# Optimization experiments

Hardware: AMD Instinct MI355X
Metric: run time of the kernel (lower is better)

Reference implementation:

```python
import jax, jax.numpy as jnp
import numpy as np

HID = 512
VOCAB = 2048
K_CB = 4


def conv1d(x, w, b, stride):
    # x: [B, C_in, L], w: [C_out, C_in, 7], torch Conv1d(k=7, stride, pad=3)
    y = jax.lax.conv_general_dilated(
        x, w, window_strides=(stride,), padding=[(3, 3)],
        dimension_numbers=("NCH", "OIH", "NCH"))
    return y + b[None, :, None]


def setup_inputs() -> dict:
    key = jax.random.key(0)
    ks = jax.random.split(key, 9)
    B, S = 4, 32768
    audio = jax.random.normal(ks[0], (B, 1, S), dtype=jnp.float32)
    # encoder params (fan-in scaled init, like torch default scale-wise)
    w1 = jax.random.normal(ks[1], (HID // 4, 1, 7), dtype=jnp.float32) * (1.0 / np.sqrt(1 * 7))
    b1 = jnp.zeros((HID // 4,), dtype=jnp.float32)
    w2 = jax.random.normal(ks[2], (HID // 2, HID // 4, 7), dtype=jnp.float32) * (1.0 / np.sqrt(HID // 4 * 7))
    b2 = jnp.zeros((HID // 2,), dtype=jnp.float32)
    w3 = jax.random.normal(ks[3], (HID, HID // 2, 7), dtype=jnp.float32) * (1.0 / np.sqrt(HID // 2 * 7))
    b3 = jnp.zeros((HID,), dtype=jnp.float32)
    codebook = jax.random.normal(ks[4], (K_CB, VOCAB, HID), dtype=jnp.float32)
    embedding = jax.random.normal(ks[5], (VOCAB, HID), dtype=jnp.float32)
    return {"audio": audio, "w1": w1, "b1": b1, "w2": w2, "b2": b2,
            "w3": w3, "b3": b3, "codebook": codebook, "embedding": embedding}


def reference(audio, w1, b1, w2, b2, w3, b3, codebook, embedding):
    # conv encoder: [B,1,S] -> [B,H,L], L = S/8
    f = jax.nn.relu(conv1d(audio, w1, b1, 2))
    f = jax.nn.relu(conv1d(f, w2, b2, 2))
    f = conv1d(f, w3, b3, 2)
    feats = jnp.transpose(f, (0, 2, 1))  # [B, L, H]

    # multi-codebook nearest neighbor: argmin of squared L2 == argmin of cdist
    f2 = jnp.sum(feats * feats, axis=-1)          # [B, L]
    c2 = jnp.sum(codebook * codebook, axis=-1)    # [K, V]
    cross = jnp.einsum("blh,kvh->bklv", feats, codebook)  # [B, K, L, V]
    d2 = f2[:, None, :, None] + c2[None, :, None, :] - 2.0 * cross
    tokens = jnp.argmin(d2, axis=-1)              # [B, K, L] (stack over codebooks at dim=1)
    emb = embedding[tokens].mean(axis=1)          # [B, L, H]
    return tokens, emb
```

## Files before the change

### kernel.cpp

```cpp
#include <hip/hip_runtime.h>
#include <hip/hip_bf16.h>
#include <stdint.h>

#define B_ 4
#define S_IN 32768
#define C1V 128
#define L1V 16384
#define C2V 256
#define L2V 8192
#define C3V 512
#define L3V 4096
#define VOCABV 2048
#define KCB 4

#define R1P (2 * (L1V + 16))
#define P1P (L1V + 16)
#define R2P (2 * (L2V + 16))
#define P2P (L2V + 16)

typedef _Float16 half8 __attribute__((ext_vector_type(8)));
typedef float floatx4 __attribute__((ext_vector_type(4)));

#define AS1 __attribute__((address_space(1)))
#define AS3 __attribute__((address_space(3)))

__device__ __forceinline__ void gload_lds16(const void* g, void* l) {
    __builtin_amdgcn_global_load_lds((const AS1 void*)g, (AS3 void*)l, 16, 0, 0);
}

__device__ __forceinline__ half8 lds_read_half8_a4(const _Float16* p) {
    union { uint32_t u[4]; half8 h; } t;
    const uint32_t* w = (const uint32_t*)p;
    t.u[0] = w[0]; t.u[1] = w[1]; t.u[2] = w[2]; t.u[3] = w[3];
    return t.h;
}

__global__ void padzero_kernel(_Float16* __restrict__ x1h, _Float16* __restrict__ x2h) {
    int j = blockIdx.x * 256 + threadIdx.x;
    half8 z;
#pragma unroll
    for (int i = 0; i < 8; ++i) z[i] = (_Float16)0.f;
    if (j < 2048) {
        int row = j >> 2, p = j & 3;
        size_t base = (size_t)row * R1P + (size_t)(p >> 1) * P1P + ((p & 1) ? (L1V + 8) : 0);
        *(half8*)(x1h + base) = z;
    } else if (j < 6144) {
        int j2 = j - 2048;
        int row = j2 >> 2, p = j2 & 3;
        size_t base = (size_t)row * R2P + (size_t)(p >> 1) * P2P + ((p & 1) ? (L2V + 8) : 0);
        *(half8*)(x2h + base) = z;
    }
}

__global__ void conv1_kernel(const float* __restrict__ x, const float* __restrict__ w,
                             const float* __restrict__ bias, _Float16* __restrict__ out) {
    __shared__ float xs[2 * 256 + 6];
    __shared__ float ws[7];
    const int l0 = blockIdx.x * 256;
    const int co = blockIdx.y;
    const int b  = blockIdx.z;
    const int tid = threadIdx.x;
    const float* xb = x + (size_t)b * S_IN;
    for (int n = tid; n < 2 * 256 + 6; n += 256) {
        int p = 2 * l0 - 3 + n;
        xs[n] = (p >= 0 && p < S_IN) ? xb[p] : 0.f;
    }
    if (tid < 7) ws[tid] = w[co * 7 + tid];
    __syncthreads();
    float acc = bias[co];
    const int base = 2 * tid;
#pragma unroll
    for (int t = 0; t < 7; ++t) acc = fmaf(ws[t], xs[base + t], acc);
    float s = fmaxf(acc, 0.f) * 1024.f;
    _Float16 h  = (_Float16)s;
    _Float16 lo = (_Float16)(s - (float)h);
    size_t o = (size_t)(b * C1V + co) * R1P + 8 + l0 + tid;
    out[o] = h;
    out[o + P1P] = lo;
}

__global__ void wsplit_kernel(const float* __restrict__ w, _Float16* __restrict__ wh,
                              _Float16* __restrict__ wl, int cin, int cout) {
    int idx = blockIdx.x * 256 + threadIdx.x;
    if (idx >= cin * cout) return;
    int co = idx / cin;
    int ci = idx - co * cin;
    const float* src = w + ((size_t)co * cin + ci) * 7;
    half8 h, l;
    h[0] = (_Float16)0.f; l[0] = (_Float16)0.f;
#pragma unroll
    for (int u = 1; u < 8; ++u) {
        float v = src[u - 1] * 1024.f;
        _Float16 hh = (_Float16)v;
        h[u] = hh;
        l[u] = (_Float16)(v - (float)hh);
    }
    size_t o = (size_t)co * (cin * 8) + ci * 8;
    *(half8*)(wh + o) = h;
    *(half8*)(wl + o) = l;
}


__global__ __launch_bounds__(256, 2) void conv2_mfma_kernel(
    const _Float16* __restrict__ xin, const _Float16* __restrict__ WH,
    const _Float16* __restrict__ WL, const float* __restrict__ bias,
    _Float16* __restrict__ xout) {
    __shared__ _Float16 Xs[2176];
    __shared__ _Float16 WsH[128 * 32], WsL[128 * 32];
    const int tid = threadIdx.x;
    const int wave = tid >> 6;
    const int lane = tid & 63;
    const int wm = wave >> 1, wn = wave & 1;
    const int q  = lane >> 4;
    const int cl = lane & 15;
    const int l0  = blockIdx.x * 128;
    const int co0 = blockIdx.y * 128;
    const int b   = blockIdx.z;

    const int wrow  = lane >> 2;
    const int wseg  = lane & 3;
    const int wsoff = (wseg ^ ((wrow >> 1) & 3)) * 8;
    const int rq    = (q ^ ((cl >> 1) & 3)) * 8;

    const int pl0 = (tid >= 136) ? 1 : 0;
    const int r0  = tid - pl0 * 136;
    const int ci0 = r0 / 34;
    const int sg0 = r0 - ci0 * 34;
    const _Float16* xb = xin + (size_t)b * C1V * R1P;

    floatx4 acc[4][4];
#pragma unroll
    for (int a = 0; a < 4; ++a)
#pragma unroll
        for (int n = 0; n < 4; ++n) acc[a][n] = (floatx4){0.f, 0.f, 0.f, 0.f};

    for (int ch = 0; ch < 32; ++ch) {
        __syncthreads();
        {
            const _Float16* gx = xb + (size_t)(ch * 4 + ci0) * R1P + pl0 * P1P + 2 * l0 + sg0 * 8;
            gload_lds16(gx, (char*)Xs + (tid & ~63) * 16);
            if (tid < 16) {
                const _Float16* gt = xb + (size_t)(ch * 4 + 3) * R1P + P1P + 2 * l0 + (18 + tid) * 8;
                gload_lds16(gt, (char*)Xs + 4096);
            }
        }
        const int k0 = ch * 32;
        for (int g = wave; g < 8; g += 4) {
            const _Float16* gh = WH + (size_t)(co0 + g * 16 + wrow) * 1024 + k0 + wsoff;
            const _Float16* gl = WL + (size_t)(co0 + g * 16 + wrow) * 1024 + k0 + wsoff;
            gload_lds16(gh, (char*)WsH + g * 1024);
            gload_lds16(gl, (char*)WsL + g * 1024);
        }
        asm volatile("s_waitcnt vmcnt(0)" ::: "memory");
        __syncthreads();

        half8 awh[4], awl[4], bxh[4], bxl[4];
#pragma unroll
        for (int a = 0; a < 4; ++a) {
            const int ro = (wm * 64 + a * 16 + cl) * 32 + rq;
            awh[a] = *(const half8*)&WsH[ro];
            awl[a] = *(const half8*)&WsL[ro];
        }
#pragma unroll
        for (int n = 0; n < 4; ++n) {
            const int lrel = wn * 64 + n * 16 + cl;
            bxh[n] = lds_read_half8_a4(&Xs[q * 272 + 4 + 2 * lrel]);
            bxl[n] = lds_read_half8_a4(&Xs[1088 + q * 272 + 4 + 2 * lrel]);
        }
#pragma unroll
        for (int a = 0; a < 4; ++a)
#pragma unroll
            for (int n = 0; n < 4; ++n) {
                acc[a][n] = __builtin_amdgcn_mfma_f32_16x16x32_f16(awh[a], bxh[n], acc[a][n], 0, 0, 0);
                acc[a][n] = __builtin_amdgcn_mfma_f32_16x16x32_f16(awl[a], bxh[n], acc[a][n], 0, 0, 0);
                acc[a][n] = __builtin_amdgcn_mfma_f32_16x16x32_f16(awh[a], bxl[n], acc[a][n], 0, 0, 0);
            }
    }

    float bv[4][4];
#pragma unroll
    for (int a = 0; a < 4; ++a)
#pragma unroll
        for (int r = 0; r < 4; ++r) bv[a][r] = bias[co0 + wm * 64 + a * 16 + q * 4 + r];
#pragma unroll
    for (int a = 0; a < 4; ++a)
#pragma unroll
        for (int n = 0; n < 4; ++n) {
            const int l = l0 + wn * 64 + n * 16 + cl;
#pragma unroll
            for (int r = 0; r < 4; ++r) {
                const int co = co0 + wm * 64 + a * 16 + q * 4 + r;
                float vv = fmaxf(acc[a][n][r] * (1.f / 1048576.f) + bv[a][r], 0.f);
                float s = vv * 1024.f;
                _Float16 h  = (_Float16)s;
                _Float16 lo = (_Float16)(s - (float)h);
                size_t o = (size_t)(b * C2V + co) * R2P + 8 + l;
                xout[o] = h;
                xout[o + P2P] = lo;
            }
        }
}

__global__ __launch_bounds__(256, 2) void conv3_mfma_kernel(
    const _Float16* __restrict__ xin, const _Float16* __restrict__ WH,
    const _Float16* __restrict__ WL, const float* __restrict__ bias,
    _Float16* __restrict__ outh) {
    __shared__ _Float16 Xs[2176];
    __shared__ _Float16 WsH[128 * 32], WsL[128 * 32];
    const int tid = threadIdx.x;
    const int wave = tid >> 6;
    const int lane = tid & 63;
    const int wm = wave >> 1, wn = wave & 1;
    const int q  = lane >> 4;
    const int cl = lane & 15;
    const int l0  = blockIdx.x * 128;
    const int co0 = blockIdx.y * 128;
    const int b   = blockIdx.z;

    const int wrow  = lane >> 2;
    const int wseg  = lane & 3;
    const int wsoff = (wseg ^ ((wrow >> 1) & 3)) * 8;
    const int rq    = (q ^ ((cl >> 1) & 3)) * 8;

    const int pl0 = (tid >= 136) ? 1 : 0;
    const int r0  = tid - pl0 * 136;
    const int ci0 = r0 / 34;
    const int sg0 = r0 - ci0 * 34;
    const _Float16* xb = xin + (size_t)b * C2V * R2P;

    floatx4 acc[4][4];
#pragma unroll
    for (int a = 0; a < 4; ++a)
#pragma unroll
        for (int n = 0; n < 4; ++n) acc[a][n] = (floatx4){0.f, 0.f, 0.f, 0.f};

    for (int ch = 0; ch < 64; ++ch) {
        __syncthreads();
        {
            const _Float16* gx = xb + (size_t)(ch * 4 + ci0) * R2P + pl0 * P2P + 2 * l0 + sg0 * 8;
            gload_lds16(gx, (char*)Xs + (tid & ~63) * 16);
            if (tid < 16) {
                const _Float16* gt = xb + (size_t)(ch * 4 + 3) * R2P + P2P + 2 * l0 + (18 + tid) * 8;
                gload_lds16(gt, (char*)Xs + 4096);
            }
        }
        const int k0 = ch * 32;
        for (int g = wave; g < 8; g += 4) {
            const _Float16* gh = WH + (size_t)(co0 + g * 16 + wrow) * 2048 + k0 + wsoff;
            const _Float16* gl = WL + (size_t)(co0 + g * 16 + wrow) * 2048 + k0 + wsoff;
            gload_lds16(gh, (char*)WsH + g * 1024);
            gload_lds16(gl, (char*)WsL + g * 1024);
        }
        asm volatile("s_waitcnt vmcnt(0)" ::: "memory");
        __syncthreads();

        half8 axh[4], axl[4], bwh[4], bwl[4];
#pragma unroll
        for (int a = 0; a < 4; ++a) {
            const int lrel = wm * 64 + a * 16 + cl;
            axh[a] = lds_read_half8_a4(&Xs[q * 272 + 4 + 2 * lrel]);
            axl[a] = lds_read_half8_a4(&Xs[1088 + q * 272 + 4 + 2 * lrel]);
        }
#pragma unroll
        for (int n = 0; n < 4; ++n) {
            const int ro = (wn * 64 + n * 16 + cl) * 32 + rq;
            bwh[n] = *(const half8*)&WsH[ro];
            bwl[n] = *(const half8*)&WsL[ro];
        }
#pragma unroll
        for (int a = 0; a < 4; ++a)
#pragma unroll
            for (int n = 0; n < 4; ++n) {
                acc[a][n] = __builtin_amdgcn_mfma_f32_16x16x32_f16(axh[a], bwh[n], acc[a][n], 0, 0, 0);
                acc[a][n] = __builtin_amdgcn_mfma_f32_16x16x32_f16(axl[a], bwh[n], acc[a][n], 0, 0, 0);
                acc[a][n] = __builtin_amdgcn_mfma_f32_16x16x32_f16(axh[a], bwl[n], acc[a][n], 0, 0, 0);
            }
    }

    float bv[4];
#pragma unroll
    for (int n = 0; n < 4; ++n) bv[n] = bias[co0 + wn * 64 + n * 16 + cl];
#pragma unroll
    for (int a = 0; a < 4; ++a)
#pragma unroll
        for (int n = 0; n < 4; ++n) {
            const int co = co0 + wn * 64 + n * 16 + cl;
#pragma unroll
            for (int r = 0; r < 4; ++r) {
                const int l = l0 + wm * 64 + a * 16 + q * 4 + r;
                float f = acc[a][n][r] * (1.f / 1048576.f) + bv[n];
                float s = f * 1024.f;
                _Float16 h = (_Float16)s;
                _Float16 lo = (_Float16)(s - (float)h);
                _Float16* dst = outh + ((size_t)b * L3V + l) * 1024 + co;
                dst[0] = h;
                dst[512] = lo;
            }
        }
}

__global__ void cbprep_kernel(const float* __restrict__ cb, _Float16* __restrict__ y,
                              float* __restrict__ c2p) {
    const int r = blockIdx.x;
    const int lane = threadIdx.x;
    const float* row = cb + (size_t)r * 512;
    float4 a = *(const float4*)&row[lane * 8];
    float4 c = *(const float4*)&row[lane * 8 + 4];
    float s = a.x * a.x + a.y * a.y + a.z * a.z + a.w * a.w
            + c.x * c.x + c.y * c.y + c.z * c.z + c.w * c.w;
#pragma unroll
    for (int off = 32; off > 0; off >>= 1) s += __shfl_down(s, off, 64);
    if (lane == 0) c2p[r] = s * 524288.f;

    const float e[8] = {a.x, a.y, a.z, a.w, c.x, c.y, c.z, c.w};
    half8 hv, lv;
#pragma unroll
    for (int i = 0; i < 8; ++i) {
        float v = e[i] * 1024.f;
        _Float16 h = (_Float16)v;
        hv[i] = h;
        lv[i] = (_Float16)(v - (float)h);
    }
    *(half8*)(y + (size_t)r * 1024 + lane * 8) = hv;
    *(half8*)(y + (size_t)r * 1024 + 512 + lane * 8) = lv;
}

__global__ __launch_bounds__(512, 2) void cross_mfma_kernel(
    const _Float16* __restrict__ Af, const _Float16* __restrict__ Bf,
    const float* __restrict__ c2p,
    int* __restrict__ tok_i, float* __restrict__ tok_f) {

    __shared__ _Float16 AsH[2][8192], AsL[2][8192];
    __shared__ _Float16 BsH[2][8192], BsL[2][8192];
    __shared__ float c2s[2048];
    __shared__ float slotv[2][256];
    __shared__ int   sloti[2][256];

    const int tid  = threadIdx.x;
    const int w    = tid >> 6;
    const int lane = tid & 63;
    const int wm = w >> 1;
    const int wn = w & 1;
    const int q  = lane >> 4;
    const int cl = lane & 15;

    const int l0 = blockIdx.x * 256;
    const int k  = blockIdx.y;
    const int b  = blockIdx.z;

    const _Float16* Ab = Af + (size_t)(b * L3V + l0) * 1024;
    const _Float16* Bb = Bf + (size_t)k * VOCABV * 1024;

    {
        float4 cv = *(const float4*)&c2p[k * VOCABV + tid * 4];
        *(float4*)&c2s[tid * 4] = cv;
    }
    if (tid < 256) {
        slotv[0][tid] = -3.4e38f; slotv[1][tid] = -3.4e38f;
        sloti[0][tid] = 0;        sloti[1][tid] = 0;
    }

    const int arow  = w * 16 + (lane >> 2);
    const int bg    = (w >> 1) & 1;
    const int bj    = (w & 1) * 16 + (lane >> 2);
    const int bpl   = w >> 2;
    const int sswz8 = ((lane & 3) ^ ((lane >> 3) & 3)) * 8;
    const int brq   = (q ^ ((cl >> 1) & 3)) * 8;

#define STAGE_A(NXT, KON, PL, H) do { \
    const _Float16* s_ = Ab + (size_t)((H) * 128 + arow) * 1024 + (PL) * 512 + (KON) + sswz8; \
    gload_lds16(s_, ((PL) ? (char*)&AsL[NXT][0] : (char*)&AsH[NXT][0]) \
                     + (H) * 8192 + w * 1024 + lane * 16); \
} while (0)
#define STAGE_B(NXT, VTN, KON, C) do { \
    const _Float16* s_ = Bb + (size_t)((VTN) * 256 + 128 * bg + 32 * (C) + bj) * 1024 \
                         + bpl * 512 + (KON) + sswz8; \
    gload_lds16(s_, (bpl ? (char*)&BsL[NXT][0] : (char*)&BsH[NXT][0]) \
                     + (C) * 4096 + (w & 3) * 1024 + lane * 16); \
} while (0)

    floatx4 acc[4][8];
    half8 ah[4], al[4];
    int cur = 0;

    STAGE_A(0, 0, 0, 0); STAGE_A(0, 0, 0, 1);
    STAGE_A(0, 0, 1, 0); STAGE_A(0, 0, 1, 1);
    STAGE_B(0, 0, 0, 0); STAGE_B(0, 0, 0, 1);
    STAGE_B(0, 0, 0, 2); STAGE_B(0, 0, 0, 3);

#define PHASE(P, VMC) do { \
    asm volatile("s_waitcnt vmcnt(" #VMC ")" ::: "memory"); \
    __builtin_amdgcn_s_barrier(); \
    if ((P) == 0) { \
        _Pragma("unroll") \
        for (int mt = 0; mt < 4; ++mt) { \
            const int aro = (wm * 64 + mt * 16 + cl) * 32 + brq; \
            ah[mt] = *(const half8*)&AsH[cur][aro]; \
            al[mt] = *(const half8*)&AsL[cur][aro]; \
        } \
    } \
    const int bro0_ = (P) * 2048 + wn * 1024 + cl * 32 + brq; \
    const int bro1_ = bro0_ + 512; \
    half8 bh0_ = *(const half8*)&BsH[cur][bro0_]; \
    half8 bl0_ = *(const half8*)&BsL[cur][bro0_]; \
    half8 bh1_ = *(const half8*)&BsH[cur][bro1_]; \
    half8 bl1_ = *(const half8*)&BsL[cur][bro1_]; \
    if ((P) == 0)      { STAGE_A(nxt, kon, 0, 0); STAGE_A(nxt, kon, 0, 1); } \
    else if ((P) == 1) { STAGE_A(nxt, kon, 1, 0); STAGE_A(nxt, kon, 1, 1); } \
    else if ((P) == 2) { STAGE_B(nxt, vtn, kon, 0); STAGE_B(nxt, vtn, kon, 1); } \
    else               { STAGE_B(nxt, vtn, kon, 2); STAGE_B(nxt, vtn, kon, 3); } \
    asm volatile("s_waitcnt lgkmcnt(0)" ::: "memory"); \
    __builtin_amdgcn_sched_barrier(0); \
    __builtin_amdgcn_s_setprio(1); \
    _Pragma("unroll") \
    for (int mt = 0; mt < 4; ++mt) { \
        acc[mt][2*(P)]   = __builtin_amdgcn_mfma_f32_16x16x32_f16(ah[mt], bh0_, acc[mt][2*(P)], 0, 0, 0); \
        acc[mt][2*(P)]   = __builtin_amdgcn_mfma_f32_16x16x32_f16(al[mt], bh0_, acc[mt][2*(P)], 0, 0, 0); \
        acc[mt][2*(P)]   = __builtin_amdgcn_mfma_f32_16x16x32_f16(ah[mt], bl0_, acc[mt][2*(P)], 0, 0, 0); \
        acc[mt][2*(P)+1] = __builtin_amdgcn_mfma_f32_16x16x32_f16(ah[mt], bh1_, acc[mt][2*(P)+1], 0, 0, 0); \
        acc[mt][2*(P)+1] = __builtin_amdgcn_mfma_f32_16x16x32_f16(al[mt], bh1_, acc[mt][2*(P)+1], 0, 0, 0); \
        acc[mt][2*(P)+1] = __builtin_amdgcn_mfma_f32_16x16x32_f16(ah[mt], bl1_, acc[mt][2*(P)+1], 0, 0, 0); \
    } \
    __builtin_amdgcn_s_setprio(0); \
    __builtin_amdgcn_sched_barrier(0); \
} while (0)

#pragma unroll 1
    for (int t = 0; t < 128; ++t) {
        const int nxt = cur ^ 1;
        const int tn  = t + 1;
        const int vtn = tn >> 4;
        const int kon = (tn & 15) << 5;
        const int vt  = t >> 4;

        if ((t & 15) == 0) {
#pragma unroll
            for (int mt = 0; mt < 4; ++mt)
#pragma unroll
                for (int nt = 0; nt < 8; ++nt) acc[mt][nt] = (floatx4){0.f, 0.f, 0.f, 0.f};
        }

        { PHASE(0, 3); }
        { PHASE(1, 4); }
        { PHASE(2, 5); }
        { PHASE(3, 6); }
        cur = nxt;

        if ((t & 15) == 15) {
            float c2v[8];
#pragma unroll
            for (int nt = 0; nt < 8; ++nt)
                c2v[nt] = c2s[vt * 256 + wn * 128 + nt * 16 + cl];
#pragma unroll
            for (int mt = 0; mt < 4; ++mt)
#pragma unroll
                for (int r = 0; r < 4; ++r) {
                    float bv = acc[mt][0][r] - c2v[0];
                    int   bi = vt * 256 + wn * 128 + cl;
#pragma unroll
                    for (int nt = 1; nt < 8; ++nt) {
                        float m = acc[mt][nt][r] - c2v[nt];
                        int   vi = vt * 256 + wn * 128 + nt * 16 + cl;
                        if (m > bv) { bv = m; bi = vi; }
                    }
#pragma unroll
                    for (int msk = 1; msk < 16; msk <<= 1) {
                        float ov = __shfl_xor(bv, msk, 64);
                        int   oi = __shfl_xor(bi, msk, 64);
                        if (ov > bv || (ov == bv && oi < bi)) { bv = ov; bi = oi; }
                    }
                    if (cl == 0) {
                        const int row = wm * 64 + mt * 16 + q * 4 + r;
                        float cur_v = slotv[wn][row];
                        int   ci  = sloti[wn][row];
                        if (bv > cur_v || (bv == cur_v && bi < ci)) {
                            slotv[wn][row] = bv;
                            sloti[wn][row] = bi;
                        }
                    }
                }
        }
    }
#undef PHASE
#undef STAGE_A
#undef STAGE_B

    __syncthreads();
    if (tid < 256) {
        float v0 = slotv[0][tid], v1 = slotv[1][tid];
        int   i0 = sloti[0][tid], i1 = sloti[1][tid];
        bool t1 = (v1 > v0);
        int best = t1 ? i1 : i0;
        const int n = (b * KCB + k) * L3V + l0 + tid;
        tok_i[n] = best;
        tok_f[n] = (float)best;
    }
}

__global__ void emb_kernel(const int* __restrict__ tokens, const float* __restrict__ E,
                           float* __restrict__ out) {
    const int l = blockIdx.x;
    const int b = blockIdx.y;
    const int h4 = threadIdx.x * 4;
    const int t0 = tokens[((size_t)(b * KCB + 0)) * L3V + l];
    const int t1 = tokens[((size_t)(b * KCB + 1)) * L3V + l];
    const int t2 = tokens[((size_t)(b * KCB + 2)) * L3V + l];
    const int t3 = tokens[((size_t)(b * KCB + 3)) * L3V + l];
    const float4 e0 = *(const float4*)&E[(size_t)t0 * 512 + h4];
    const float4 e1 = *(const float4*)&E[(size_t)t1 * 512 + h4];
    const float4 e2 = *(const float4*)&E[(size_t)t2 * 512 + h4];
    const float4 e3 = *(const float4*)&E[(size_t)t3 * 512 + h4];
    float4 r;
    r.x = (e0.x + e1.x + e2.x + e3.x) * 0.25f;
    r.y = (e0.y + e1.y + e2.y + e3.y) * 0.25f;
    r.z = (e0.z + e1.z + e2.z + e3.z) * 0.25f;
    r.w = (e0.w + e1.w + e2.w + e3.w) * 0.25f;
    *(float4*)&out[((size_t)b * L3V + l) * 512 + h4] = r;
}

extern "C" void kernel_launch(void* const* d_in, const int* in_sizes, int n_in,
                              void* d_out, int out_size, void* d_ws, size_t ws_size,
                              hipStream_t stream) {
    const float* audio = (const float*)d_in[0];
    const float* w1 = (const float*)d_in[1];
    const float* b1 = (const float*)d_in[2];
    const float* w2 = (const float*)d_in[3];
    const float* b2 = (const float*)d_in[4];
    const float* w3 = (const float*)d_in[5];
    const float* b3 = (const float*)d_in[6];
    const float* cb = (const float*)d_in[7];
    const float* E  = (const float*)d_in[8];

    float* out_tok = (float*)d_out;
    float* out_emb = out_tok + (size_t)B_ * KCB * L3V;

    float* ws = (float*)d_ws;
    size_t off = 0;
    float* x1f = ws + off; off += (size_t)B_ * C1V * (L1V + 16);
    float* x2f = ws + off; off += (size_t)B_ * C2V * (L2V + 16);
    float* w2h_f = ws + off; off += (size_t)C2V * (C1V * 8) / 2;
    float* w2l_f = ws + off; off += (size_t)C2V * (C1V * 8) / 2;
    float* w3h_f = ws + off; off += (size_t)C3V * (C2V * 8) / 2;
    float* w3l_f = ws + off; off += (size_t)C3V * (C2V * 8) / 2;
    float* c2p = ws + off; off += (size_t)KCB * VOCABV;
    int*   tok = (int*)(ws + off); off += (size_t)B_ * KCB * L3V;

    _Float16* X1  = (_Float16*)x1f;
    _Float16* X2  = (_Float16*)x2f;
    _Float16* Afh = (_Float16*)x1f;
    _Float16* Bfh = (_Float16*)x2f;
    _Float16* W2H = (_Float16*)w2h_f; _Float16* W2L = (_Float16*)w2l_f;
    _Float16* W3H = (_Float16*)w3h_f; _Float16* W3L = (_Float16*)w3l_f;

    padzero_kernel<<<24, 256, 0, stream>>>(X1, X2);

    wsplit_kernel<<<(C2V * C1V + 255) / 256, 256, 0, stream>>>(w2, W2H, W2L, C1V, C2V);
    wsplit_kernel<<<(C3V * C2V + 255) / 256, 256, 0, stream>>>(w3, W3H, W3L, C2V, C3V);

    conv1_kernel<<<dim3(L1V / 256, C1V, B_), 256, 0, stream>>>(audio, w1, b1, X1);

    conv2_mfma_kernel<<<dim3(L2V / 128, C2V / 128, B_), 256, 0, stream>>>(
        X1, W2H, W2L, b2, X2);

    conv3_mfma_kernel<<<dim3(L3V / 128, C3V / 128, B_), 256, 0, stream>>>(
        X2, W3H, W3L, b3, Afh);

    cbprep_kernel<<<KCB * VOCABV, 64, 0, stream>>>(cb, Bfh, c2p);

    cross_mfma_kernel<<<dim3(L3V / 256, KCB, B_), 512, 0, stream>>>(
        Afh, Bfh, c2p, tok, out_tok);

    emb_kernel<<<dim3(L3V, B_), 128, 0, stream>>>(tok, E, out_emb);
}
```

Measured before the change: 595.7 us.

## Collapse four per-phase barriers into one and prefetch B fragments across MFMA chunks

The main codebook-distance GEMM loop now issues all global-to-LDS staging for the next tile at the start of each iteration, behind a single vmcnt(0) wait and one barrier, instead of four phases that each waited and synchronized. LDS reads of the B fragments are double-buffered in registers so the next chunk's reads overlap the current chunk's MFMAs, and staging is skipped on the last iteration. This is meant to cut barrier and wait overhead and to hide LDS latency behind MFMA work. In exchange it uses more registers, and the full vmcnt(0) wait may expose global load latency if an iteration is too short to cover it.

```diff
diff --git a/kernel.cpp b/kernel.cpp
--- a/kernel.cpp
+++ b/kernel.cpp
@@ -378,52 +378,41 @@
     gload_lds16(s_, (bpl ? (char*)&BsL[NXT][0] : (char*)&BsH[NXT][0]) \
                      + (C) * 4096 + (w & 3) * 1024 + lane * 16); \
 } while (0)
-
-    floatx4 acc[4][8];
-    half8 ah[4], al[4];
-    int cur = 0;
-
-    STAGE_A(0, 0, 0, 0); STAGE_A(0, 0, 0, 1);
-    STAGE_A(0, 0, 1, 0); STAGE_A(0, 0, 1, 1);
-    STAGE_B(0, 0, 0, 0); STAGE_B(0, 0, 0, 1);
-    STAGE_B(0, 0, 0, 2); STAGE_B(0, 0, 0, 3);
-
-#define PHASE(P, VMC) do { \
-    asm volatile("s_waitcnt vmcnt(" #VMC ")" ::: "memory"); \
-    __builtin_amdgcn_s_barrier(); \
-    if ((P) == 0) { \
-        _Pragma("unroll") \
-        for (int mt = 0; mt < 4; ++mt) { \
-            const int aro = (wm * 64 + mt * 16 + cl) * 32 + brq; \
-            ah[mt] = *(const half8*)&AsH[cur][aro]; \
-            al[mt] = *(const half8*)&AsL[cur][aro]; \
-        } \
-    } \
-    const int bro0_ = (P) * 2048 + wn * 1024 + cl * 32 + brq; \
-    const int bro1_ = bro0_ + 512; \
-    half8 bh0_ = *(const half8*)&BsH[cur][bro0_]; \
-    half8 bl0_ = *(const half8*)&BsL[cur][bro0_]; \
-    half8 bh1_ = *(const half8*)&BsH[cur][bro1_]; \
-    half8 bl1_ = *(const half8*)&BsL[cur][bro1_]; \
-    if ((P) == 0)      { STAGE_A(nxt, kon, 0, 0); STAGE_A(nxt, kon, 0, 1); } \
-    else if ((P) == 1) { STAGE_A(nxt, kon, 1, 0); STAGE_A(nxt, kon, 1, 1); } \
-    else if ((P) == 2) { STAGE_B(nxt, vtn, kon, 0); STAGE_B(nxt, vtn, kon, 1); } \
-    else               { STAGE_B(nxt, vtn, kon, 2); STAGE_B(nxt, vtn, kon, 3); } \
-    asm volatile("s_waitcnt lgkmcnt(0)" ::: "memory"); \
-    __builtin_amdgcn_sched_barrier(0); \
+#define STAGE_ALL(NXT, VTN, KON) do { \
+    STAGE_A(NXT, KON, 0, 0); STAGE_A(NXT, KON, 0, 1); \
+    STAGE_A(NXT, KON, 1, 0); STAGE_A(NXT, KON, 1, 1); \
+    STAGE_B(NXT, VTN, KON, 0); STAGE_B(NXT, VTN, KON, 1); \
+    STAGE_B(NXT, VTN, KON, 2); STAGE_B(NXT, VTN, KON, 3); \
+} while (0)
+
+#define READ_B(P, H0, L0, H1, L1) do { \
+    const int bro_ = (P) * 2048 + wn * 1024 + cl * 32 + brq; \
+    H0 = *(const half8*)&BsH[cur][bro_]; \
+    L0 = *(const half8*)&BsL[cur][bro_]; \
+    H1 = *(const half8*)&BsH[cur][bro_ + 512]; \
+    L1 = *(const half8*)&BsL[cur][bro_ + 512]; \
+} while (0)
+
+#define MFMA_CHUNK(P, H0, L0, H1, L1) do { \
     __builtin_amdgcn_s_setprio(1); \
     _Pragma("unroll") \
     for (int mt = 0; mt < 4; ++mt) { \
-        acc[mt][2*(P)]   = __builtin_amdgcn_mfma_f32_16x16x32_f16(ah[mt], bh0_, acc[mt][2*(P)], 0, 0, 0); \
-        acc[mt][2*(P)]   = __builtin_amdgcn_mfma_f32_16x16x32_f16(al[mt], bh0_, acc[mt][2*(P)], 0, 0, 0); \
-        acc[mt][2*(P)]   = __builtin_amdgcn_mfma_f32_16x16x32_f16(ah[mt], bl0_, acc[mt][2*(P)], 0, 0, 0); \
-        acc[mt][2*(P)+1] = __builtin_amdgcn_mfma_f32_16x16x32_f16(ah[mt], bh1_, acc[mt][2*(P)+1], 0, 0, 0); \
-        acc[mt][2*(P)+1] = __builtin_amdgcn_mfma_f32_16x16x32_f16(al[mt], bh1_, acc[mt][2*(P)+1], 0, 0, 0); \
-        acc[mt][2*(P)+1] = __builtin_amdgcn_mfma_f32_16x16x32_f16(ah[mt], bl1_, acc[mt][2*(P)+1], 0, 0, 0); \
+        acc[mt][2*(P)]   = __builtin_amdgcn_mfma_f32_16x16x32_f16(ah[mt], H0, acc[mt][2*(P)], 0, 0, 0); \
+        acc[mt][2*(P)]   = __builtin_amdgcn_mfma_f32_16x16x32_f16(al[mt], H0, acc[mt][2*(P)], 0, 0, 0); \
+        acc[mt][2*(P)]   = __builtin_amdgcn_mfma_f32_16x16x32_f16(ah[mt], L0, acc[mt][2*(P)], 0, 0, 0); \
+        acc[mt][2*(P)+1] = __builtin_amdgcn_mfma_f32_16x16x32_f16(ah[mt], H1, acc[mt][2*(P)+1], 0, 0, 0); \
+        acc[mt][2*(P)+1] = __builtin_amdgcn_mfma_f32_16x16x32_f16(al[mt], H1, acc[mt][2*(P)+1], 0, 0, 0); \
+        acc[mt][2*(P)+1] = __builtin_amdgcn_mfma_f32_16x16x32_f16(ah[mt], L1, acc[mt][2*(P)+1], 0, 0, 0); \
     } \
     __builtin_amdgcn_s_setprio(0); \
     __builtin_amdgcn_sched_barrier(0); \
 } while (0)
+
+    floatx4 acc[4][8];
+    half8 ah[4], al[4];
+    int cur = 0;
+
+    STAGE_ALL(0, 0, 0);
 
 #pragma unroll 1
     for (int t = 0; t < 128; ++t) {
@@ -440,10 +429,30 @@
                 for (int nt = 0; nt < 8; ++nt) acc[mt][nt] = (floatx4){0.f, 0.f, 0.f, 0.f};
         }
 
-        { PHASE(0, 3); }
-        { PHASE(1, 4); }
-        { PHASE(2, 5); }
-        { PHASE(3, 6); }
+        asm volatile("s_waitcnt vmcnt(0)" ::: "memory");
+        __builtin_amdgcn_s_barrier();
+        if (t < 127) STAGE_ALL(nxt, vtn, kon);
+        __builtin_amdgcn_sched_barrier(0);
+
+#pragma unroll
+        for (int mt = 0; mt < 4; ++mt) {
+            const int aro = (wm * 64 + mt * 16 + cl) * 32 + brq;
+            ah[mt] = *(const half8*)&AsH[cur][aro];
+            al[mt] = *(const half8*)&AsL[cur][aro];
+        }
+        half8 b0h0, b0l0, b0h1, b0l1, b1h0, b1l0, b1h1, b1l1;
+        READ_B(0, b0h0, b0l0, b0h1, b0l1);
+        READ_B(1, b1h0, b1l0, b1h1, b1l1);
+        __builtin_amdgcn_sched_barrier(0);
+
+        MFMA_CHUNK(0, b0h0, b0l0, b0h1, b0l1);
+        READ_B(2, b0h0, b0l0, b0h1, b0l1);
+        __builtin_amdgcn_sched_barrier(0);
+        MFMA_CHUNK(1, b1h0, b1l0, b1h1, b1l1);
+        READ_B(3, b1h0, b1l0, b1h1, b1l1);
+        __builtin_amdgcn_sched_barrier(0);
+        MFMA_CHUNK(2, b0h0, b0l0, b0h1, b0l1);
+        MFMA_CHUNK(3, b1h0, b1l0, b1h1, b1l1);
         cur = nxt;
 
         if ((t & 15) == 15) {
@@ -481,7 +490,9 @@
                 }
         }
     }
-#undef PHASE
+#undef MFMA_CHUNK
+#undef READ_B
+#undef STAGE_ALL
 #undef STAGE_A
 #undef STAGE_B
 
```

Result: slower. 636.3 us (+6.8%).
